# Kernel optimization log

Hardware: AMD Instinct MI355X
Metric: run time of the kernel (lower is better)

## Reference

```python
import jax, jax.numpy as jnp
import numpy as np

DIM = 1536
NHEADS = 12
HDIM = DIM // NHEADS  # 128
EPS = 1e-6
LOCAL_ATTN_SIZE = 3
SINK_SIZE = 1
MAX_ATTN = 32760 if LOCAL_ATTN_SIZE == -1 else LOCAL_ATTN_SIZE * 1560  # 4680


def _rms(x, g):
    # WanRMSNorm over last dim
    return x * jax.lax.rsqrt(jnp.mean(x * x, axis=-1, keepdims=True) + EPS) * g


def _rope(x, f, h, w, fr, fi, start_frame):
    # x: [b, s, n, d] with s == f*h*w; fr/fi: [1024, d//2] real/imag of complex rotations
    b, s, n, d = x.shape
    c = d // 2
    c0 = c - 2 * (c // 3)
    c1 = c // 3
    fc = jax.lax.complex(fr, fi)  # [1024, c]
    xr = x.reshape(b, s, n, c, 2)
    xc = jax.lax.complex(xr[..., 0], xr[..., 1])  # [b, s, n, c]
    ff = fc[start_frame:start_frame + f, :c0]      # [f, c0]
    fh = fc[:h, c0:c0 + c1]                        # [h, c1]
    fw = fc[:w, c0 + c1:c0 + 2 * c1]               # [w, c1]
    freqs_i = jnp.concatenate([
        jnp.broadcast_to(ff[:, None, None, :], (f, h, w, c0)),
        jnp.broadcast_to(fh[None, :, None, :], (f, h, w, c1)),
        jnp.broadcast_to(fw[None, None, :, :], (f, h, w, c1)),
    ], axis=-1).reshape(1, s, 1, c)
    y = xc * freqs_i
    return jnp.stack([y.real, y.imag], axis=-1).reshape(b, s, n, d)


def _attn(q, k, v):
    # plain SDPA (decode path of the module uses no mask on the gathered window)
    scale = 1.0 / np.sqrt(q.shape[-1]).astype(np.float32)
    logits = jnp.einsum('bqnd,bknd->bnqk', q, k) * scale
    p = jax.nn.softmax(logits, axis=-1)
    return jnp.einsum('bnqk,bknd->bqnd', p, v)


def _forward(x, cache_k, cache_v, freqs_real, freqs_imag,
             wq, bq, wk, bk, wv, bv, wo, bo, gq, gk,
             f_frames, height, width, current_start, global_end_index, local_end_index):
    b, s, _ = x.shape
    n, d = NHEADS, HDIM
    frame_seqlen = height * width
    start_frame = current_start // frame_seqlen

    q = _rms(x @ wq + bq, gq).reshape(b, s, n, d)
    k = _rms(x @ wk + bk, gk).reshape(b, s, n, d)
    v = (x @ wv + bv).reshape(b, s, n, d)

    rq = _rope(q, f_frames, height, width, freqs_real, freqs_imag, start_frame)
    rk = _rope(k, f_frames, height, width, freqs_real, freqs_imag, start_frame)

    current_end = current_start + s
    sink_tokens = SINK_SIZE * frame_seqlen
    kv_size = cache_k.shape[1]
    is_recompute = (current_end <= global_end_index) and (current_start > 0)

    kc, vc = cache_k, cache_v
    if LOCAL_ATTN_SIZE != -1 and current_end > global_end_index and s + local_end_index > kv_size:
        # evict oldest non-sink tokens, roll the rest toward the sink region
        num_evicted = s + local_end_index - kv_size
        num_rolled = local_end_index - num_evicted - sink_tokens
        src = slice(sink_tokens + num_evicted, sink_tokens + num_evicted + num_rolled)
        kc = kc.at[:, sink_tokens:sink_tokens + num_rolled].set(jax.lax.stop_gradient(cache_k[:, src]))
        vc = vc.at[:, sink_tokens:sink_tokens + num_rolled].set(jax.lax.stop_gradient(cache_v[:, src]))
        new_local_end = local_end_index + current_end - global_end_index - num_evicted
    else:
        new_local_end = local_end_index + current_end - global_end_index
    local_start = new_local_end - s
    write_start = max(local_start, sink_tokens) if is_recompute else local_start
    off = max(0, write_start - local_start)
    wl = max(0, new_local_end - write_start)
    if wl > 0:
        kc = kc.at[:, write_start:new_local_end].set(rk[:, off:off + wl])
        vc = vc.at[:, write_start:new_local_end].set(v[:, off:off + wl])

    if sink_tokens > 0:
        budget = MAX_ATTN - sink_tokens
        if budget > 0:
            lo = max(sink_tokens, new_local_end - budget)
            kcat = jnp.concatenate([kc[:, :sink_tokens], kc[:, lo:new_local_end]], axis=1)
            vcat = jnp.concatenate([vc[:, :sink_tokens], vc[:, lo:new_local_end]], axis=1)
        else:
            kcat, vcat = kc[:, :sink_tokens], vc[:, :sink_tokens]
        o = _attn(rq, kcat, vcat)
    else:
        ws = max(0, new_local_end - MAX_ATTN)
        o = _attn(rq, kc[:, ws:new_local_end], vc[:, ws:new_local_end])

    return o.reshape(b, s, DIM) @ wo + bo


def setup_inputs() -> dict:
    key = jax.random.key(0)
    ks = jax.random.split(key, 12)
    B, S, CACHE = 1, 1560, 4680
    sc = 0.02
    # RoPE tables as unit-magnitude complex rotations
    ang = jax.random.uniform(ks[0], (1024, HDIM // 2), jnp.float32, 0.0, 2.0 * np.pi)
    return {
        'x': jax.random.normal(ks[1], (B, S, DIM), jnp.float32),
        'cache_k': jax.random.normal(ks[2], (B, CACHE, NHEADS, HDIM), jnp.float32),
        'cache_v': jax.random.normal(ks[3], (B, CACHE, NHEADS, HDIM), jnp.float32),
        'freqs_real': jnp.cos(ang),
        'freqs_imag': jnp.sin(ang),
        'wq': jax.random.normal(ks[4], (DIM, DIM), jnp.float32) * sc,
        'bq': jnp.zeros((DIM,), jnp.float32),
        'wk': jax.random.normal(ks[5], (DIM, DIM), jnp.float32) * sc,
        'bk': jnp.zeros((DIM,), jnp.float32),
        'wv': jax.random.normal(ks[6], (DIM, DIM), jnp.float32) * sc,
        'bv': jnp.zeros((DIM,), jnp.float32),
        'wo': jax.random.normal(ks[7], (DIM, DIM), jnp.float32) * sc,
        'bo': jnp.zeros((DIM,), jnp.float32),
        'gq': jnp.ones((DIM,), jnp.float32),
        'gk': jnp.ones((DIM,), jnp.float32),
        'f_frames': 1,
        'height': 30,
        'width': 52,
        'current_start': 4680,
        'global_end_index': 4680,
        'local_end_index': 4680,
    }


def reference(x, cache_k, cache_v, freqs_real, freqs_imag,
              wq, bq, wk, bk, wv, bv, wo, bo, gq, gk,
              f_frames, height, width, current_start, global_end_index, local_end_index):
    return _forward(x, cache_k, cache_v, freqs_real, freqs_imag,
                    wq, bq, wk, bk, wv, bv, wo, bo, gq, gk,
                    f_frames, height, width, current_start, global_end_index, local_end_index)
```

## Files before the change

### kernel.cpp

```cpp
#include <hip/hip_runtime.h>
#include <cstdint>
#include <cstddef>

typedef unsigned int  u32;
typedef unsigned short u16;
typedef short s16x8 __attribute__((ext_vector_type(8)));
typedef float f32x4 __attribute__((ext_vector_type(4)));

#define DIM     1536
#define NH      12
#define HD      128
#define SEQ     1560
#define MPAD    1664
#define NKV     4680
#define NKPAD   4736
#define ROLL0   3120
#define NQK     4608
#define START_FRAME 3
#define NEGINF  -3.0e4f
#define NSPLIT  3
#define SPLITKC 1600

__device__ __forceinline__ u16 f2bf(float f){
  u32 u = __builtin_bit_cast(u32, f);
  u32 r = (u + 0x7fffu + ((u >> 16) & 1u)) >> 16;
  return (u16)r;
}

__global__ void k_zero_pads(u16* __restrict__ Kc, u16* __restrict__ VT,
                            u16* __restrict__ Qr, u16* __restrict__ Opad){
  int i = blockIdx.x * 256 + threadIdx.x;
  uint4 z = make_uint4(0u, 0u, 0u, 0u);
  if (i < 10752){
    int h = i / 896, r = i % 896;
    ((uint4*)(Kc + ((size_t)h * NKPAD + NKV) * 128))[r] = z;
  } else if (i < 21504){
    int j = i - 10752; int row = j / 7, c = j % 7;
    ((uint4*)(VT + (size_t)row * NKPAD + NKV))[c] = z;
  } else if (i < 41472){
    int j = i - 21504; int h = j / 1664, r = j % 1664;
    ((uint4*)(Qr + ((size_t)h * MPAD + SEQ) * 128))[r] = z;
  } else if (i < 61440){
    int r = i - 41472;
    ((uint4*)(Opad + (size_t)SEQ * DIM))[r] = z;
  }
}

__global__ void k_prep_x(const float* __restrict__ x, u16* __restrict__ xp){
  int i = blockIdx.x * 256 + threadIdx.x;
  const int n_src = SEQ * DIM / 8;
  u16 o[8] = {0,0,0,0,0,0,0,0};
  if (i < n_src){
    float4 a = ((const float4*)x)[2*i];
    float4 b = ((const float4*)x)[2*i + 1];
    o[0]=f2bf(a.x); o[1]=f2bf(a.y); o[2]=f2bf(a.z); o[3]=f2bf(a.w);
    o[4]=f2bf(b.x); o[5]=f2bf(b.y); o[6]=f2bf(b.z); o[7]=f2bf(b.w);
  }
  uint4 v = make_uint4((u32)o[0]|((u32)o[1]<<16), (u32)o[2]|((u32)o[3]<<16),
                       (u32)o[4]|((u32)o[5]<<16), (u32)o[6]|((u32)o[7]<<16));
  ((uint4*)xp)[i] = v;
}

__global__ void k_transpose_w(const float* __restrict__ wq, const float* __restrict__ wk,
                              const float* __restrict__ wv, const float* __restrict__ wo,
                              u16* __restrict__ WT){
  __shared__ u32 tile[64][65];
  int z = blockIdx.z;
  const float* w = (z==0)?wq:(z==1)?wk:(z==2)?wv:wo;
  u16* dst = WT + (size_t)z * DIM * DIM;
  int r0 = blockIdx.x * 64, c0 = blockIdx.y * 64;
  int t = threadIdx.x;
  int rr = t >> 4, cg = t & 15;
#pragma unroll
  for (int i = 0; i < 4; i++){
    int r = rr + i * 16;
    float4 v = *(const float4*)(w + (size_t)(r0 + r) * DIM + c0 + cg * 4);
    tile[r][cg*4+0] = f2bf(v.x); tile[r][cg*4+1] = f2bf(v.y);
    tile[r][cg*4+2] = f2bf(v.z); tile[r][cg*4+3] = f2bf(v.w);
  }
  __syncthreads();
  int c = t >> 2, rg = t & 3;
  u32 wds[8];
#pragma unroll
  for (int j = 0; j < 8; j++)
    wds[j] = (tile[rg*16 + 2*j][c] & 0xffffu) | (tile[rg*16 + 2*j + 1][c] << 16);
  u16* q = dst + (size_t)(c0 + c) * DIM + r0 + rg * 16;
  *(uint4*)q       = make_uint4(wds[0], wds[1], wds[2], wds[3]);
  *(uint4*)(q + 8) = make_uint4(wds[4], wds[5], wds[6], wds[7]);
}

#define LDK 40
__global__ __launch_bounds__(256) void k_gemm_qkv(
    const u16* __restrict__ A, const u16* __restrict__ B,
    const float* __restrict__ biasq, const float* __restrict__ biask, const float* __restrict__ biasv,
    float* __restrict__ Y, float* __restrict__ sumsq){
  __shared__ u16 As[128*LDK];
  __shared__ u16 Bs[128*LDK];
  int m0 = blockIdx.y * 128, n0 = blockIdx.x * 128;
  int t = threadIdx.x, w = t >> 6, lane = t & 63, quad = lane >> 4, lc = lane & 15;
  int wm = w & 1, wn = w >> 1;
  int sr = t >> 1, sh = (t & 1) * 16;
  f32x4 acc[4][4] = {};
  for (int kt = 0; kt < DIM/32; kt++){
    int k0 = kt * 32;
    __syncthreads();
    {
      const uint4* ga = (const uint4*)(A + (size_t)(m0 + sr) * DIM + k0 + sh);
      uint4 a0 = ga[0], a1 = ga[1];
      const uint4* gb = (const uint4*)(B + (size_t)(n0 + sr) * DIM + k0 + sh);
      uint4 b0 = gb[0], b1 = gb[1];
      *(uint4*)(As + sr * LDK + sh)     = a0;
      *(uint4*)(As + sr * LDK + sh + 8) = a1;
      *(uint4*)(Bs + sr * LDK + sh)     = b0;
      *(uint4*)(Bs + sr * LDK + sh + 8) = b1;
    }
    __syncthreads();
    s16x8 af[4], bf[4];
#pragma unroll
    for (int mt = 0; mt < 4; mt++) af[mt] = *(const s16x8*)(As + (wm*64 + mt*16 + lc) * LDK + quad * 8);
#pragma unroll
    for (int nt = 0; nt < 4; nt++) bf[nt] = *(const s16x8*)(Bs + (wn*64 + nt*16 + lc) * LDK + quad * 8);
#pragma unroll
    for (int mt = 0; mt < 4; mt++)
#pragma unroll
      for (int nt = 0; nt < 4; nt++)
        acc[mt][nt] = __builtin_amdgcn_mfma_f32_16x16x32_bf16(af[mt], bf[nt], acc[mt][nt], 0, 0, 0);
  }
  const float* bias; int cbase; int which;
  if (n0 < DIM)        { bias = biasq; cbase = 0;     which = 0; }
  else if (n0 < 2*DIM) { bias = biask; cbase = DIM;   which = 1; }
  else                 { bias = biasv; cbase = 2*DIM; which = 2; }
  float bvals[4];
#pragma unroll
  for (int nt = 0; nt < 4; nt++) bvals[nt] = bias[n0 - cbase + wn*64 + nt*16 + lc];
#pragma unroll
  for (int mt = 0; mt < 4; mt++){
    int row0 = m0 + wm*64 + mt*16 + quad*4;
    float ss[4] = {0.f, 0.f, 0.f, 0.f};
#pragma unroll
    for (int nt = 0; nt < 4; nt++){
      int col = n0 + wn*64 + nt*16 + lc;
#pragma unroll
      for (int r = 0; r < 4; r++){
        float y = acc[mt][nt][r] + bvals[nt];
        Y[(size_t)(row0 + r) * NQK + col] = y;
        ss[r] += y * y;
      }
    }
    if (which < 2){
      float* dst = sumsq + (which ? MPAD : 0);
#pragma unroll
      for (int r = 0; r < 4; r++){
        float v = ss[r];
        v += __shfl_xor(v, 1); v += __shfl_xor(v, 2); v += __shfl_xor(v, 4); v += __shfl_xor(v, 8);
        if (lc == 0) atomicAdd(&dst[row0 + r], v);
      }
    }
  }
}

__global__ void k_rope_qk(const float* __restrict__ Y, const float* __restrict__ sumsq,
                          const float* __restrict__ gq, const float* __restrict__ gk,
                          const float* __restrict__ fre, const float* __restrict__ fim,
                          u16* __restrict__ Qr, u16* __restrict__ Kc){
  int pos = blockIdx.x;
  int t = threadIdx.x;
  float scq = rsqrtf(sumsq[pos]        * (1.0f/1536.0f) + 1e-6f);
  float sck = rsqrtf(sumsq[MPAD + pos] * (1.0f/1536.0f) + 1e-6f);
  int hrow = pos / 52, wrow = pos % 52;
#pragma unroll
  for (int i = 0; i < 3; i++){
    int p = t + i * 256;
    int head = p >> 6, j = p & 63;
    int frow = (j < 22) ? START_FRAME : ((j < 43) ? hrow : wrow);
    float cr = fre[frow * 64 + j], ci = fim[frow * 64 + j];
    int d0 = head * 128 + 2 * j;
    float2 yq = *(const float2*)(Y + (size_t)pos * NQK + d0);
    float qa = yq.x * scq * gq[d0];
    float qb = yq.y * scq * gq[d0 + 1];
    u32 oq = (u32)f2bf(qa * cr - qb * ci) | ((u32)f2bf(qa * ci + qb * cr) << 16);
    *(u32*)(Qr + (size_t)(head * MPAD + pos) * 128 + 2 * j) = oq;
    float2 yk = *(const float2*)(Y + (size_t)pos * NQK + DIM + d0);
    float ka = yk.x * sck * gk[d0];
    float kb = yk.y * sck * gk[d0 + 1];
    u32 ok = (u32)f2bf(ka * cr - kb * ci) | ((u32)f2bf(ka * ci + kb * cr) << 16);
    *(u32*)(Kc + (size_t)(head * NKPAD + ROLL0 + pos) * 128 + 2 * j) = ok;
  }
}

__global__ void k_copy_cache_k(const float* __restrict__ ck, u16* __restrict__ Kc){
  int p = blockIdx.x;
  int src = (p < SEQ) ? p : p + SEQ;
  int t = threadIdx.x;
  int h = t >> 4, d = (t & 15) * 8;
  const float* s = ck + (size_t)src * DIM + t * 8;
  float4 a = ((const float4*)s)[0], b = ((const float4*)s)[1];
  uint4 v = make_uint4((u32)f2bf(a.x)|((u32)f2bf(a.y)<<16), (u32)f2bf(a.z)|((u32)f2bf(a.w)<<16),
                       (u32)f2bf(b.x)|((u32)f2bf(b.y)<<16), (u32)f2bf(b.z)|((u32)f2bf(b.w)<<16));
  *(uint4*)(Kc + (size_t)(h * NKPAD + p) * 128 + d) = v;
}

__global__ void k_tv_cache(const float* __restrict__ cv, u16* __restrict__ VT){
  __shared__ u32 tile[64][65];
  int p0 = blockIdx.x * 64, hd0 = blockIdx.y * 64;
  int t = threadIdx.x;
  int pr = t >> 4, cg = t & 15;
#pragma unroll
  for (int i = 0; i < 4; i++){
    int p = p0 + pr + i * 16;
    if (p < ROLL0){
      int src = (p < SEQ) ? p : p + SEQ;
      float4 v = *(const float4*)(cv + (size_t)src * DIM + hd0 + cg * 4);
      tile[pr + i*16][cg*4+0] = f2bf(v.x); tile[pr + i*16][cg*4+1] = f2bf(v.y);
      tile[pr + i*16][cg*4+2] = f2bf(v.z); tile[pr + i*16][cg*4+3] = f2bf(v.w);
    }
  }
  __syncthreads();
  int hd = t >> 2, pg = t & 3;
  int pbase = p0 + pg * 16;
  if (pbase < ROLL0){
    u32 wds[8];
#pragma unroll
    for (int j = 0; j < 8; j++)
      wds[j] = (tile[pg*16 + 2*j][hd] & 0xffffu) | (tile[pg*16 + 2*j + 1][hd] << 16);
    u16* q = VT + (size_t)(hd0 + hd) * NKPAD + pbase;
    *(uint4*)q       = make_uint4(wds[0], wds[1], wds[2], wds[3]);
    *(uint4*)(q + 8) = make_uint4(wds[4], wds[5], wds[6], wds[7]);
  }
}

__global__ void k_tv_new(const float* __restrict__ Y, u16* __restrict__ VT){
  __shared__ u32 tile[64][65];
  int p0 = blockIdx.x * 64, hd0 = blockIdx.y * 64;
  int t = threadIdx.x;
  int pr = t >> 4, cg = t & 15;
#pragma unroll
  for (int i = 0; i < 4; i++){
    int p = p0 + pr + i * 16;
    if (p < SEQ){
      float4 v = *(const float4*)(Y + (size_t)p * NQK + 2*DIM + hd0 + cg * 4);
      tile[pr + i*16][cg*4+0] = f2bf(v.x); tile[pr + i*16][cg*4+1] = f2bf(v.y);
      tile[pr + i*16][cg*4+2] = f2bf(v.z); tile[pr + i*16][cg*4+3] = f2bf(v.w);
    }
  }
  __syncthreads();
  int hd = t >> 2, pg = t & 3;
  int pbase = p0 + pg * 16;
  u32 wds[8];
#pragma unroll
  for (int j = 0; j < 8; j++)
    wds[j] = (tile[pg*16 + 2*j][hd] & 0xffffu) | (tile[pg*16 + 2*j + 1][hd] << 16);
  u16* q = VT + (size_t)(hd0 + hd) * NKPAD + ROLL0 + pbase;
  if (pbase + 8  <= SEQ) *(uint4*)q       = make_uint4(wds[0], wds[1], wds[2], wds[3]);
  if (pbase + 16 <= SEQ) *(uint4*)(q + 8) = make_uint4(wds[4], wds[5], wds[6], wds[7]);
}

#define LDKS 136
#define LDVS 72
__global__ __launch_bounds__(256) void k_attn(const u16* __restrict__ Qr, const u16* __restrict__ Kc,
                                              const u16* __restrict__ VT,
                                              float* __restrict__ Opart, float* __restrict__ ml){
  __shared__ u16 Ks[64 * LDKS];
  __shared__ u16 Vs[128 * LDVS];
  __shared__ u16 Ps[4][16 * LDVS];
  int h = blockIdx.y, qb = blockIdx.x, sp = blockIdx.z;
  int t = threadIdx.x, w = t >> 6, lane = t & 63, quad = lane >> 4, lc = lane & 15;
  int qbase = qb * 64 + w * 16;
  const u16* Qbase = Qr + (size_t)(h * MPAD + qbase + lc) * 128;
  s16x8 qf[4];
#pragma unroll
  for (int kk = 0; kk < 4; kk++) qf[kk] = *(const s16x8*)(Qbase + kk * 32 + quad * 8);
  f32x4 oacc[8] = {};
  float m_[4] = {NEGINF, NEGINF, NEGINF, NEGINF};
  float l_[4] = {0.f, 0.f, 0.f, 0.f};
  const float scale = 0.08838834764831845f;
  const u16* Kh = Kc + (size_t)h * NKPAD * 128;
  const u16* Vh = VT + (size_t)h * 128 * NKPAD;
  u16* Pw = &Ps[w][0];
  int kr = t >> 2, kg = (t & 3) * 4;
  int vr = t >> 1, vg = (t & 1) * 4;

  int kc0 = sp * SPLITKC;
  int kc1 = (sp == NSPLIT-1) ? NKPAD : kc0 + SPLITKC;
  for (int kc = kc0; kc < kc1; kc += 64){
    __syncthreads();
    {
      const u16* ksrc = Kh + (size_t)(kc + kr) * 128 + kg * 8;
      u16* kdst = Ks + kr * LDKS + kg * 8;
      *(uint4*)(kdst)      = *(const uint4*)(ksrc);
      *(uint4*)(kdst + 8)  = *(const uint4*)(ksrc + 8);
      *(uint4*)(kdst + 16) = *(const uint4*)(ksrc + 16);
      *(uint4*)(kdst + 24) = *(const uint4*)(ksrc + 24);
      const u16* vsrc = Vh + (size_t)vr * NKPAD + kc + vg * 8;
      u16* vdst = Vs + vr * LDVS + vg * 8;
      *(uint4*)(vdst)      = *(const uint4*)(vsrc);
      *(uint4*)(vdst + 8)  = *(const uint4*)(vsrc + 8);
      *(uint4*)(vdst + 16) = *(const uint4*)(vsrc + 16);
      *(uint4*)(vdst + 24) = *(const uint4*)(vsrc + 24);
    }
    __syncthreads();
    float s[4][4];
#pragma unroll
    for (int nt = 0; nt < 4; nt++){
      f32x4 acc = {};
      int p = nt * 16 + lc;
#pragma unroll
      for (int kk = 0; kk < 4; kk++){
        s16x8 bfr = *(const s16x8*)(Ks + p * LDKS + (kk * 4 + quad) * 8);
        acc = __builtin_amdgcn_mfma_f32_16x16x32_bf16(qf[kk], bfr, acc, 0, 0, 0);
      }
#pragma unroll
      for (int r = 0; r < 4; r++) s[nt][r] = acc[r] * scale;
    }
    if (kc + 64 > NKV){
#pragma unroll
      for (int nt = 0; nt < 4; nt++){
        int col = kc + nt * 16 + lc;
        if (col >= NKV){
#pragma unroll
          for (int r = 0; r < 4; r++) s[nt][r] = NEGINF;
        }
      }
    }
    float mn[4], alpha[4];
#pragma unroll
    for (int r = 0; r < 4; r++){
      float mx = fmaxf(fmaxf(s[0][r], s[1][r]), fmaxf(s[2][r], s[3][r]));
      mx = fmaxf(mx, __shfl_xor(mx, 1)); mx = fmaxf(mx, __shfl_xor(mx, 2));
      mx = fmaxf(mx, __shfl_xor(mx, 4)); mx = fmaxf(mx, __shfl_xor(mx, 8));
      mn[r] = fmaxf(m_[r], mx);
      alpha[r] = __expf(m_[r] - mn[r]);
      m_[r] = mn[r];
    }
    float pp[4][4];
#pragma unroll
    for (int nt = 0; nt < 4; nt++)
#pragma unroll
      for (int r = 0; r < 4; r++) pp[nt][r] = __expf(s[nt][r] - mn[r]);
#pragma unroll
    for (int r = 0; r < 4; r++){
      float sum = pp[0][r] + pp[1][r] + pp[2][r] + pp[3][r];
      sum += __shfl_xor(sum, 1); sum += __shfl_xor(sum, 2);
      sum += __shfl_xor(sum, 4); sum += __shfl_xor(sum, 8);
      l_[r] = l_[r] * alpha[r] + sum;
    }
#pragma unroll
    for (int dt = 0; dt < 8; dt++){
      f32x4 oo = oacc[dt];
#pragma unroll
      for (int r = 0; r < 4; r++) oo[r] *= alpha[r];
      oacc[dt] = oo;
    }
#pragma unroll
    for (int nt = 0; nt < 4; nt++)
#pragma unroll
      for (int r = 0; r < 4; r++){
        int row = quad * 4 + r;
        Pw[row * LDVS + nt * 16 + lc] = f2bf(pp[nt][r]);
      }
    asm volatile("s_waitcnt lgkmcnt(0)" ::: "memory");
    s16x8 a0 = *(const s16x8*)(Pw + lc * LDVS + quad * 8);
    s16x8 a1 = *(const s16x8*)(Pw + lc * LDVS + 32 + quad * 8);
#pragma unroll
    for (int dt = 0; dt < 8; dt++){
      int d = dt * 16 + lc;
      s16x8 v0 = *(const s16x8*)(Vs + d * LDVS + quad * 8);
      s16x8 v1 = *(const s16x8*)(Vs + d * LDVS + 32 + quad * 8);
      oacc[dt] = __builtin_amdgcn_mfma_f32_16x16x32_bf16(a0, v0, oacc[dt], 0, 0, 0);
      oacc[dt] = __builtin_amdgcn_mfma_f32_16x16x32_bf16(a1, v1, oacc[dt], 0, 0, 0);
    }
  }
  float* Ob = Opart + ((size_t)(sp * NH + h) * MPAD) * 128;
  float* mlb = ml + ((size_t)(sp * NH + h) * MPAD) * 2;
#pragma unroll
  for (int dt = 0; dt < 8; dt++)
#pragma unroll
    for (int r = 0; r < 4; r++){
      int row = qbase + quad * 4 + r;
      Ob[(size_t)row * 128 + dt * 16 + lc] = oacc[dt][r];
    }
  if (lc == 0){
#pragma unroll
    for (int r = 0; r < 4; r++){
      int row = qbase + quad * 4 + r;
      mlb[row * 2 + 0] = m_[r];
      mlb[row * 2 + 1] = l_[r];
    }
  }
}

__global__ void k_attn_cmb(const float* __restrict__ Opart, const float* __restrict__ ml,
                           u16* __restrict__ Og){
  int row = blockIdx.x, h = blockIdx.y, d = threadIdx.x;
  float m0 = ml[((size_t)(0 * NH + h) * MPAD + row) * 2 + 0];
  float l0 = ml[((size_t)(0 * NH + h) * MPAD + row) * 2 + 1];
  float m1 = ml[((size_t)(1 * NH + h) * MPAD + row) * 2 + 0];
  float l1 = ml[((size_t)(1 * NH + h) * MPAD + row) * 2 + 1];
  float m2 = ml[((size_t)(2 * NH + h) * MPAD + row) * 2 + 0];
  float l2 = ml[((size_t)(2 * NH + h) * MPAD + row) * 2 + 1];
  float M = fmaxf(fmaxf(m0, m1), m2);
  float w0 = __expf(m0 - M), w1 = __expf(m1 - M), w2 = __expf(m2 - M);
  float L = w0 * l0 + w1 * l1 + w2 * l2;
  float o0 = Opart[((size_t)(0 * NH + h) * MPAD + row) * 128 + d];
  float o1 = Opart[((size_t)(1 * NH + h) * MPAD + row) * 128 + d];
  float o2 = Opart[((size_t)(2 * NH + h) * MPAD + row) * 128 + d];
  float o = (w0 * o0 + w1 * o1 + w2 * o2) / L;
  Og[(size_t)row * DIM + h * 128 + d] = f2bf(o);
}

__global__ __launch_bounds__(256) void k_gemm_out(const u16* __restrict__ A, const u16* __restrict__ B,
                                                  const float* __restrict__ bo, float* __restrict__ out){
  __shared__ u16 As[128*LDK];
  __shared__ u16 Bs[128*LDK];
  int m0 = blockIdx.y * 128, n0 = blockIdx.x * 128;
  int t = threadIdx.x, w = t >> 6, lane = t & 63, quad = lane >> 4, lc = lane & 15;
  int wm = w & 1, wn = w >> 1;
  int sr = t >> 1, sh = (t & 1) * 16;
  f32x4 acc[4][4] = {};
  for (int kt = 0; kt < DIM/32; kt++){
    int k0 = kt * 32;
    __syncthreads();
    {
      const uint4* ga = (const uint4*)(A + (size_t)(m0 + sr) * DIM + k0 + sh);
      uint4 a0 = ga[0], a1 = ga[1];
      const uint4* gb = (const uint4*)(B + (size_t)(n0 + sr) * DIM + k0 + sh);
      uint4 b0 = gb[0], b1 = gb[1];
      *(uint4*)(As + sr * LDK + sh)     = a0;
      *(uint4*)(As + sr * LDK + sh + 8) = a1;
      *(uint4*)(Bs + sr * LDK + sh)     = b0;
      *(uint4*)(Bs + sr * LDK + sh + 8) = b1;
    }
    __syncthreads();
    s16x8 af[4], bf[4];
#pragma unroll
    for (int mt = 0; mt < 4; mt++) af[mt] = *(const s16x8*)(As + (wm*64 + mt*16 + lc) * LDK + quad * 8);
#pragma unroll
    for (int nt = 0; nt < 4; nt++) bf[nt] = *(const s16x8*)(Bs + (wn*64 + nt*16 + lc) * LDK + quad * 8);
#pragma unroll
    for (int mt = 0; mt < 4; mt++)
#pragma unroll
      for (int nt = 0; nt < 4; nt++)
        acc[mt][nt] = __builtin_amdgcn_mfma_f32_16x16x32_bf16(af[mt], bf[nt], acc[mt][nt], 0, 0, 0);
  }
  float bvals[4];
#pragma unroll
  for (int nt = 0; nt < 4; nt++) bvals[nt] = bo[n0 + wn*64 + nt*16 + lc];
#pragma unroll
  for (int mt = 0; mt < 4; mt++){
    int row0 = m0 + wm*64 + mt*16 + quad*4;
#pragma unroll
    for (int nt = 0; nt < 4; nt++){
      int col = n0 + wn*64 + nt*16 + lc;
#pragma unroll
      for (int r = 0; r < 4; r++){
        int row = row0 + r;
        if (row < SEQ) out[(size_t)row * DIM + col] = acc[mt][nt][r] + bvals[nt];
      }
    }
  }
}

extern "C" void kernel_launch(void* const* d_in, const int* in_sizes, int n_in,
                              void* d_out, int out_size, void* d_ws, size_t ws_size,
                              hipStream_t stream){
  const float* x   = (const float*)d_in[0];
  const float* ck  = (const float*)d_in[1];
  const float* cv  = (const float*)d_in[2];
  const float* fre = (const float*)d_in[3];
  const float* fim = (const float*)d_in[4];
  const float* wq  = (const float*)d_in[5];
  const float* bq  = (const float*)d_in[6];
  const float* wk  = (const float*)d_in[7];
  const float* bk  = (const float*)d_in[8];
  const float* wv  = (const float*)d_in[9];
  const float* bv  = (const float*)d_in[10];
  const float* wo  = (const float*)d_in[11];
  const float* bo  = (const float*)d_in[12];
  const float* gq  = (const float*)d_in[13];
  const float* gk  = (const float*)d_in[14];

  char* ws = (char*)d_ws;
  size_t off = 0;
  u16*   xpad  = (u16*)(ws + off);  off += (size_t)MPAD * DIM * 2;
  u16*   WT    = (u16*)(ws + off);  off += (size_t)4 * DIM * DIM * 2;
  float* Y     = (float*)(ws + off); off += (size_t)MPAD * NQK * 4;
  float* sumsq = (float*)(ws + off); off += (size_t)2 * MPAD * 4;
  u16*   Qr    = (u16*)(ws + off);  off += (size_t)NH * MPAD * 128 * 2;
  u16*   Kc    = (u16*)(ws + off);  off += (size_t)NH * NKPAD * 128 * 2;
  u16*   VT    = (u16*)(ws + off);  off += (size_t)NH * 128 * NKPAD * 2;
  u16*   Opad  = (u16*)(ws + off);  off += (size_t)MPAD * DIM * 2;
  if (off > ws_size) return;
  float* Opart = Y;
  float* ml    = (float*)xpad;

  hipMemsetAsync(sumsq, 0, (size_t)2 * MPAD * 4, stream);
  k_zero_pads   <<<dim3(240), 256, 0, stream>>>(Kc, VT, Qr, Opad);
  k_prep_x      <<<dim3(MPAD*DIM/8/256), 256, 0, stream>>>(x, xpad);
  k_transpose_w <<<dim3(24, 24, 4), 256, 0, stream>>>(wq, wk, wv, wo, WT);
  k_gemm_qkv    <<<dim3(NQK/128, MPAD/128), 256, 0, stream>>>(xpad, WT, bq, bk, bv, Y, sumsq);
  k_rope_qk     <<<dim3(SEQ), 256, 0, stream>>>(Y, sumsq, gq, gk, fre, fim, Qr, Kc);
  k_copy_cache_k<<<dim3(ROLL0), 192, 0, stream>>>(ck, Kc);
  k_tv_cache    <<<dim3(49, 24), 256, 0, stream>>>(cv, VT);
  k_tv_new      <<<dim3(25, 24), 256, 0, stream>>>(Y, VT);
  k_attn        <<<dim3(26, NH, NSPLIT), 256, 0, stream>>>(Qr, Kc, VT, Opart, ml);
  k_attn_cmb    <<<dim3(SEQ, NH), 128, 0, stream>>>(Opart, ml, Opad);
  k_gemm_out    <<<dim3(DIM/128, MPAD/128), 256, 0, stream>>>(Opad, WT + (size_t)3*DIM*DIM, bo, (float*)d_out);
}
```

Measured before the change: 420.4 us.

## Double the attention block to 128 queries and register-prefetch next K/V tile

The attention kernel now runs 512-thread blocks covering 128 query rows, so each K/V tile loaded into shared memory is reused by twice as many waves. The next tile's K and V are fetched into registers right after the barrier and stored to shared memory at the start of the next iteration, so global load latency overlaps the MFMA and softmax work. The grid is halved in the x dimension. The cost is fewer blocks in flight and extra registers per thread, with launch bounds asking for 4 blocks per CU.

```diff
diff --git a/kernel.cpp b/kernel.cpp
--- a/kernel.cpp
+++ b/kernel.cpp
@@ -257,15 +257,15 @@
 
 #define LDKS 136
 #define LDVS 72
-__global__ __launch_bounds__(256) void k_attn(const u16* __restrict__ Qr, const u16* __restrict__ Kc,
-                                              const u16* __restrict__ VT,
-                                              float* __restrict__ Opart, float* __restrict__ ml){
+__global__ __launch_bounds__(512, 4) void k_attn(const u16* __restrict__ Qr, const u16* __restrict__ Kc,
+                                                 const u16* __restrict__ VT,
+                                                 float* __restrict__ Opart, float* __restrict__ ml){
   __shared__ u16 Ks[64 * LDKS];
   __shared__ u16 Vs[128 * LDVS];
-  __shared__ u16 Ps[4][16 * LDVS];
+  __shared__ u16 Ps[8][16 * LDVS];
   int h = blockIdx.y, qb = blockIdx.x, sp = blockIdx.z;
   int t = threadIdx.x, w = t >> 6, lane = t & 63, quad = lane >> 4, lc = lane & 15;
-  int qbase = qb * 64 + w * 16;
+  int qbase = qb * 128 + w * 16;
   const u16* Qbase = Qr + (size_t)(h * MPAD + qbase + lc) * 128;
   s16x8 qf[4];
 #pragma unroll
@@ -277,28 +277,35 @@
   const u16* Kh = Kc + (size_t)h * NKPAD * 128;
   const u16* Vh = VT + (size_t)h * 128 * NKPAD;
   u16* Pw = &Ps[w][0];
-  int kr = t >> 2, kg = (t & 3) * 4;
-  int vr = t >> 1, vg = (t & 1) * 4;
+  int kr0 = t >> 4,          kg0 = (t & 15) * 8;
+  int kr1 = (t + 512) >> 4,  kg1 = ((t + 512) & 15) * 8;
+  int vd0 = t >> 3,          vp0 = (t & 7) * 8;
+  int vd1 = (t + 512) >> 3,  vp1 = ((t + 512) & 7) * 8;
 
   int kc0 = sp * SPLITKC;
   int kc1 = (sp == NSPLIT-1) ? NKPAD : kc0 + SPLITKC;
+  uint4 kp0, kp1, vp0r, vp1r;
+  {
+    int kc = kc0;
+    kp0  = *(const uint4*)(Kh + (size_t)(kc + kr0) * 128 + kg0);
+    kp1  = *(const uint4*)(Kh + (size_t)(kc + kr1) * 128 + kg1);
+    vp0r = *(const uint4*)(Vh + (size_t)vd0 * NKPAD + kc + vp0);
+    vp1r = *(const uint4*)(Vh + (size_t)vd1 * NKPAD + kc + vp1);
+  }
   for (int kc = kc0; kc < kc1; kc += 64){
     __syncthreads();
-    {
-      const u16* ksrc = Kh + (size_t)(kc + kr) * 128 + kg * 8;
-      u16* kdst = Ks + kr * LDKS + kg * 8;
-      *(uint4*)(kdst)      = *(const uint4*)(ksrc);
-      *(uint4*)(kdst + 8)  = *(const uint4*)(ksrc + 8);
-      *(uint4*)(kdst + 16) = *(const uint4*)(ksrc + 16);
-      *(uint4*)(kdst + 24) = *(const uint4*)(ksrc + 24);
-      const u16* vsrc = Vh + (size_t)vr * NKPAD + kc + vg * 8;
-      u16* vdst = Vs + vr * LDVS + vg * 8;
-      *(uint4*)(vdst)      = *(const uint4*)(vsrc);
-      *(uint4*)(vdst + 8)  = *(const uint4*)(vsrc + 8);
-      *(uint4*)(vdst + 16) = *(const uint4*)(vsrc + 16);
-      *(uint4*)(vdst + 24) = *(const uint4*)(vsrc + 24);
-    }
+    *(uint4*)(Ks + kr0 * LDKS + kg0) = kp0;
+    *(uint4*)(Ks + kr1 * LDKS + kg1) = kp1;
+    *(uint4*)(Vs + vd0 * LDVS + vp0) = vp0r;
+    *(uint4*)(Vs + vd1 * LDVS + vp1) = vp1r;
     __syncthreads();
+    if (kc + 64 < kc1){
+      int kn = kc + 64;
+      kp0  = *(const uint4*)(Kh + (size_t)(kn + kr0) * 128 + kg0);
+      kp1  = *(const uint4*)(Kh + (size_t)(kn + kr1) * 128 + kg1);
+      vp0r = *(const uint4*)(Vh + (size_t)vd0 * NKPAD + kn + vp0);
+      vp1r = *(const uint4*)(Vh + (size_t)vd1 * NKPAD + kn + vp1);
+    }
     float s[4][4];
 #pragma unroll
     for (int nt = 0; nt < 4; nt++){
@@ -332,14 +339,13 @@
       alpha[r] = __expf(m_[r] - mn[r]);
       m_[r] = mn[r];
     }
-    float pp[4][4];
 #pragma unroll
     for (int nt = 0; nt < 4; nt++)
 #pragma unroll
-      for (int r = 0; r < 4; r++) pp[nt][r] = __expf(s[nt][r] - mn[r]);
+      for (int r = 0; r < 4; r++) s[nt][r] = __expf(s[nt][r] - mn[r]);
 #pragma unroll
     for (int r = 0; r < 4; r++){
-      float sum = pp[0][r] + pp[1][r] + pp[2][r] + pp[3][r];
+      float sum = s[0][r] + s[1][r] + s[2][r] + s[3][r];
       sum += __shfl_xor(sum, 1); sum += __shfl_xor(sum, 2);
       sum += __shfl_xor(sum, 4); sum += __shfl_xor(sum, 8);
       l_[r] = l_[r] * alpha[r] + sum;
@@ -356,7 +362,7 @@
 #pragma unroll
       for (int r = 0; r < 4; r++){
         int row = quad * 4 + r;
-        Pw[row * LDVS + nt * 16 + lc] = f2bf(pp[nt][r]);
+        Pw[row * LDVS + nt * 16 + lc] = f2bf(s[nt][r]);
       }
     asm volatile("s_waitcnt lgkmcnt(0)" ::: "memory");
     s16x8 a0 = *(const s16x8*)(Pw + lc * LDVS + quad * 8);
@@ -502,7 +508,7 @@
   k_copy_cache_k<<<dim3(ROLL0), 192, 0, stream>>>(ck, Kc);
   k_tv_cache    <<<dim3(49, 24), 256, 0, stream>>>(cv, VT);
   k_tv_new      <<<dim3(25, 24), 256, 0, stream>>>(Y, VT);
-  k_attn        <<<dim3(26, NH, NSPLIT), 256, 0, stream>>>(Qr, Kc, VT, Opart, ml);
+  k_attn        <<<dim3(MPAD/128, NH, NSPLIT), 512, 0, stream>>>(Qr, Kc, VT, Opart, ml);
   k_attn_cmb    <<<dim3(SEQ, NH), 128, 0, stream>>>(Opart, ml, Opad);
   k_gemm_out    <<<dim3(DIM/128, MPAD/128), 256, 0, stream>>>(Opad, WT + (size_t)3*DIM*DIM, bo, (float*)d_out);
 }
```

After: 392.4 us. 1.07x faster.
